# Kernel optimization log

Hardware: AMD Instinct MI355X
Metric: run time of the kernel (lower is better)

The kernel has to match this reference:

```python
import jax, jax.numpy as jnp
import numpy as np

N = 50000      # nodes
E = 800000     # edges (before self-loops)
H = 4          # attention heads
C = 64         # hidden_dim per head
F_IN = 8       # node_features
NEG_SLOPE = 0.2  # PyG GATConv default


def setup_inputs() -> dict:
    key = jax.random.key(0)
    ks = jax.random.split(key, 16)
    def g(k, shape, fan_in):
        return (jax.random.normal(k, shape, jnp.float32) / np.sqrt(fan_in)).astype(jnp.float32)
    x = jax.random.normal(ks[0], (N, F_IN), jnp.float32)
    edge_index = jax.random.randint(ks[1], (2, E), 0, N, dtype=jnp.int32)
    # GATConv params: layer 0 maps F_IN->H*C, layers 1,2 map H*C->H*C
    W0 = g(ks[2], (F_IN, H * C), F_IN)
    Ws = g(ks[3], (2, H * C, H * C), H * C)
    att_src = g(ks[4], (3, H, C), C)
    att_dst = g(ks[5], (3, H, C), C)
    bconv = jnp.zeros((3, H * C), jnp.float32)
    # order / time predictor MLPs: Linear(256,64) -> ReLU -> Linear(64,1)
    ow1 = g(ks[6], (H * C, C), H * C); ob1 = jnp.zeros((C,), jnp.float32)
    ow2 = g(ks[7], (C, 1), C);         ob2 = jnp.zeros((1,), jnp.float32)
    tw1 = g(ks[8], (H * C, C), H * C); tb1 = jnp.zeros((C,), jnp.float32)
    tw2 = g(ks[9], (C, 1), C);         tb2 = jnp.zeros((1,), jnp.float32)
    return {"x": x, "edge_index": edge_index, "W0": W0, "Ws": Ws,
            "att_src": att_src, "att_dst": att_dst, "bconv": bconv,
            "ow1": ow1, "ob1": ob1, "ow2": ow2, "ob2": ob2,
            "tw1": tw1, "tb1": tb1, "tw2": tw2, "tb2": tb2}


def _gat_layer(h_in, src, dst, W, a_src, a_dst, b):
    """PyG-style GATConv (concat heads, eval mode, self-loops already in src/dst)."""
    h = (h_in @ W).reshape(N, H, C)                       # [N,H,C]
    al_s = jnp.einsum('nhc,hc->nh', h, a_src)             # [N,H]
    al_d = jnp.einsum('nhc,hc->nh', h, a_dst)             # [N,H]
    e = jax.nn.leaky_relu(al_s[src] + al_d[dst], NEG_SLOPE)  # [Etot,H]
    m = jax.ops.segment_max(e, dst, num_segments=N)       # segment-softmax over in-edges
    ee = jnp.exp(e - m[dst])
    den = jax.ops.segment_sum(ee, dst, num_segments=N)
    alpha = ee / den[dst]                                 # [Etot,H]
    out = jax.ops.segment_sum(h[src] * alpha[:, :, None], dst, num_segments=N)
    return out.reshape(N, H * C) + b


def reference(x, edge_index, W0, Ws, att_src, att_dst, bconv,
              ow1, ob1, ow2, ob2, tw1, tb1, tw2, tb2):
    loops = jnp.arange(N, dtype=edge_index.dtype)
    src = jnp.concatenate([edge_index[0], loops])
    dst = jnp.concatenate([edge_index[1], loops])
    h = _gat_layer(x, src, dst, W0, att_src[0], att_dst[0], bconv[0])
    h = jax.nn.relu(h)   # dropout is identity in eval
    h = _gat_layer(h, src, dst, Ws[0], att_src[1], att_dst[1], bconv[1])
    h = jax.nn.relu(h)
    h = _gat_layer(h, src, dst, Ws[1], att_src[2], att_dst[2], bconv[2])
    order_scores = jax.nn.relu(h @ ow1 + ob1) @ ow2 + ob2  # [N,1]
    time_scores = jax.nn.relu(h @ tw1 + tb1) @ tw2 + tb2   # [N,1]
    return (order_scores, time_scores)
```

## Files before the change

### kernel.cpp

```cpp
#include <hip/hip_runtime.h>
#include <hip/hip_bf16.h>
#include <hip/hip_fp16.h>

#define NN 50000
#define EE 800000
#define ET 850000
#define HH 4
#define CC 64
#define HC 256

using f16v8 = __attribute__((ext_vector_type(8))) _Float16;
using f32v4 = __attribute__((ext_vector_type(4))) float;

__device__ __forceinline__ float4 cvt_h4(uint2 raw) {
    __half2 a = *reinterpret_cast<__half2*>(&raw.x);
    __half2 b = *reinterpret_cast<__half2*>(&raw.y);
    float2 fa = __half22float2(a), fb = __half22float2(b);
    return make_float4(fa.x, fa.y, fb.x, fb.y);
}

#define HISTB 3321
__global__ void k_hist_prep(const int* __restrict__ ei, int* __restrict__ cnt,
                            const float* __restrict__ Ws,
                            const float* __restrict__ ow1, const float* __restrict__ tw1,
                            __half* __restrict__ Wt, __half* __restrict__ Wh) {
    if (blockIdx.x < HISTB) {
        int e = blockIdx.x * 256 + threadIdx.x;
        if (e < ET) {
            int d = (e < EE) ? ei[EE + e] : (e - EE);
            atomicAdd(&cnt[d], 1);
        }
        return;
    }
    int i = (blockIdx.x - HISTB) * 256 + threadIdx.x;
    if (i < 2 * HC * HC) {
        int m = i >> 16;
        int n = (i >> 8) & 255;
        int k = i & 255;
        Wt[i] = __float2half(Ws[m * HC * HC + k * HC + n]);
    }
    int j = i - 2 * HC * HC;
    if (j >= 0 && j < 128 * HC) {
        int c = j >> 8;
        int k = j & 255;
        float v = (c < 64) ? ow1[k * CC + c] : tw1[k * CC + (c - 64)];
        Wh[j] = __float2half(v);
    }
}

#define ASSIGNB 196
#define G0_NODES 16
__global__ __launch_bounds__(256) void k_assign_gemm0(
        const int* __restrict__ cnt, int* __restrict__ row_ptr,
        int* __restrict__ cur, int* __restrict__ cursor,
        const float* __restrict__ x, const float* __restrict__ W0,
        const float* __restrict__ asrc, const float* __restrict__ adst,
        __half* __restrict__ hg, float* __restrict__ al_s,
        float* __restrict__ al_d) {
    if (blockIdx.x < ASSIGNB) {
        int d = blockIdx.x * 256 + threadIdx.x;
        if (d < NN) {
            int off = atomicAdd(cursor, cnt[d]);
            row_ptr[d] = off;
            cur[d] = off;
        }
        return;
    }
    __shared__ float sx[G0_NODES * 8];
    int t = threadIdx.x;
    int n0 = (blockIdx.x - ASSIGNB) * G0_NODES;
    float w[8];
#pragma unroll
    for (int k = 0; k < 8; k++) w[k] = W0[k * HC + t];
    float as = asrc[t], ad = adst[t];
    int lane = t & 63, wv = t >> 6;
    if (t < G0_NODES * 8) sx[t] = x[(size_t)n0 * 8 + t];
    __syncthreads();
    for (int ni = 0; ni < G0_NODES; ni++) {
        int n = n0 + ni;
        float acc = 0.f;
#pragma unroll
        for (int k = 0; k < 8; k++) acc += sx[ni * 8 + k] * w[k];
        hg[(size_t)n * HC + t] = __float2half(acc);
        float s = acc * as, d = acc * ad;
        for (int off = 32; off > 0; off >>= 1) {
            s += __shfl_down(s, off, 64);
            d += __shfl_down(d, off, 64);
        }
        if (lane == 0) { al_s[n * HH + wv] = s; al_d[n * HH + wv] = d; }
    }
}

__global__ void k_scatter(const int* __restrict__ ei, int* __restrict__ cur,
                          unsigned short* __restrict__ esrc) {
    int e = blockIdx.x * blockDim.x + threadIdx.x;
    if (e < ET) {
        int d, s;
        if (e < EE) { d = ei[EE + e]; s = ei[e]; }
        else        { d = e - EE;     s = d; }
        int pos = atomicAdd(&cur[d], 1);
        esrc[pos] = (unsigned short)s;
    }
}

#define GM 128
#define GN 128
#define GK 64
__global__ __launch_bounds__(256) void k_gemmh(const __half* __restrict__ A,
                                               const __half* __restrict__ Bt,
                                               const float* __restrict__ asrc,
                                               const float* __restrict__ adst,
                                               __half* __restrict__ hg,
                                               float* __restrict__ al_s,
                                               float* __restrict__ al_d) {
    __shared__ __half As[GM][GK + 8];
    __shared__ __half Bs[GN][GK + 8];
    int t = threadIdx.x;
    int l = t & 63, wv = t >> 6;
    int wm = wv >> 1, wn = wv & 1;
    int row0 = blockIdx.x * GM;
    int col0 = blockIdx.y * GN;
    f32v4 acc[4][4] = {};
    const __half* Ab = A + (size_t)row0 * HC;
    const __half* Bb = Bt + (size_t)col0 * HC;
    int sr = t >> 3, sc = (t & 7) * 8;
    for (int k0 = 0; k0 < HC; k0 += GK) {
#pragma unroll
        for (int i = 0; i < 4; i++) {
            int rr = sr + i * 32;
            uint4 v = {0u, 0u, 0u, 0u};
            if (row0 + rr < NN) v = *(const uint4*)(Ab + (size_t)rr * HC + k0 + sc);
            *(uint4*)&As[rr][sc] = v;
            *(uint4*)&Bs[rr][sc] = *(const uint4*)(Bb + (size_t)rr * HC + k0 + sc);
        }
        __syncthreads();
#pragma unroll
        for (int kk = 0; kk < GK; kk += 32) {
            f16v8 af[4], bf[4];
#pragma unroll
            for (int i = 0; i < 4; i++)
                af[i] = *(const f16v8*)&As[wm * 64 + i * 16 + (l & 15)][kk + (l >> 4) * 8];
#pragma unroll
            for (int j = 0; j < 4; j++)
                bf[j] = *(const f16v8*)&Bs[wn * 64 + j * 16 + (l & 15)][kk + (l >> 4) * 8];
#pragma unroll
            for (int i = 0; i < 4; i++)
#pragma unroll
                for (int j = 0; j < 4; j++)
                    acc[i][j] = __builtin_amdgcn_mfma_f32_16x16x32_f16(af[i], bf[j], acc[i][j], 0, 0, 0);
        }
        __syncthreads();
    }
    int head = (col0 >> 6) + wn;
    float va[4], vd[4];
#pragma unroll
    for (int j = 0; j < 4; j++) {
        int c = j * 16 + (l & 15);
        va[j] = asrc[head * CC + c];
        vd[j] = adst[head * CC + c];
    }
    int cbase = col0 + wn * 64 + (l & 15);
#pragma unroll
    for (int i = 0; i < 4; i++) {
#pragma unroll
        for (int v = 0; v < 4; v++) {
            int r = row0 + wm * 64 + i * 16 + (l >> 4) * 4 + v;
            bool ok = (r < NN);
            float s = 0.f, d = 0.f;
#pragma unroll
            for (int j = 0; j < 4; j++) {
                float xv = acc[i][j][v];
                s += xv * va[j];
                d += xv * vd[j];
                if (ok) hg[(size_t)r * HC + cbase + j * 16] = __float2half(xv);
            }
            s += __shfl_xor(s, 8, 16); d += __shfl_xor(d, 8, 16);
            s += __shfl_xor(s, 4, 16); d += __shfl_xor(d, 4, 16);
            s += __shfl_xor(s, 2, 16); d += __shfl_xor(d, 2, 16);
            s += __shfl_xor(s, 1, 16); d += __shfl_xor(d, 1, 16);
            if (ok && (l & 15) == 0) {
                al_s[r * HH + head] = s;
                al_d[r * HH + head] = d;
            }
        }
    }
}

__global__ __launch_bounds__(256) void k_fagg(const int* __restrict__ cnt,
                                              const int* __restrict__ row_ptr,
                                              const unsigned short* __restrict__ esrc,
                                              const float* __restrict__ al_s,
                                              const float* __restrict__ al_d,
                                              const __half* __restrict__ hg,
                                              const float* __restrict__ bias,
                                              __half* __restrict__ out, int do_relu) {
    __shared__ float s_p[4][HH][72];
    __shared__ int   s_src[4][64];
    int t = threadIdx.x;
    int wv = t >> 6, l = t & 63;
    int n = blockIdx.x * 4 + wv;
    int myh = l >> 4;
    int beg = row_ptr[n];
    int end = beg + cnt[n];
    float4 ad = *(const float4*)&al_d[(size_t)n * HH];
    float den = 0.f;
    float4 acc = {0.f, 0.f, 0.f, 0.f};
    const __half* hgl = hg + l * 4;

    for (int off = beg; off < end; off += 64) {
        int csize = min(64, end - off);
        float4 pp = {0.f, 0.f, 0.f, 0.f};
        int s = 0;
        if (l < csize) {
            s = (int)esrc[(size_t)off + l];
            float4 as = *(const float4*)&al_s[(size_t)s * HH];
            float v;
            v = as.x + ad.x; pp.x = __expf((v > 0.f) ? v : 0.2f * v);
            v = as.y + ad.y; pp.y = __expf((v > 0.f) ? v : 0.2f * v);
            v = as.z + ad.z; pp.z = __expf((v > 0.f) ? v : 0.2f * v);
            v = as.w + ad.w; pp.w = __expf((v > 0.f) ? v : 0.2f * v);
        }
        s_src[wv][l] = s;
        s_p[wv][0][l] = pp.x;
        s_p[wv][1][l] = pp.y;
        s_p[wv][2][l] = pp.z;
        s_p[wv][3][l] = pp.w;
        const float* prow = s_p[wv][myh];
        const int*   srow = s_src[wv];
        int k = 0;
        for (; k + 8 <= csize; k += 8) {
            int si[8];
#pragma unroll
            for (int u = 0; u < 8; u++) si[u] = srow[k + u];
            uint2 rw[8];
#pragma unroll
            for (int u = 0; u < 8; u++) rw[u] = *(const uint2*)&hgl[(size_t)si[u] * HC];
            float p[8];
#pragma unroll
            for (int u = 0; u < 8; u++) p[u] = prow[k + u];
#pragma unroll
            for (int u = 0; u < 8; u++) {
                float4 v = cvt_h4(rw[u]);
                den += p[u];
                acc.x += p[u] * v.x;
                acc.y += p[u] * v.y;
                acc.z += p[u] * v.z;
                acc.w += p[u] * v.w;
            }
        }
        for (; k + 4 <= csize; k += 4) {
            int si[4];
#pragma unroll
            for (int u = 0; u < 4; u++) si[u] = srow[k + u];
            uint2 rw[4];
#pragma unroll
            for (int u = 0; u < 4; u++) rw[u] = *(const uint2*)&hgl[(size_t)si[u] * HC];
            float p[4];
#pragma unroll
            for (int u = 0; u < 4; u++) p[u] = prow[k + u];
#pragma unroll
            for (int u = 0; u < 4; u++) {
                float4 v = cvt_h4(rw[u]);
                den += p[u];
                acc.x += p[u] * v.x;
                acc.y += p[u] * v.y;
                acc.z += p[u] * v.z;
                acc.w += p[u] * v.w;
            }
        }
        for (; k < csize; k++) {
            float p = prow[k];
            float4 v = cvt_h4(*(const uint2*)&hgl[(size_t)srow[k] * HC]);
            den += p;
            acc.x += p * v.x; acc.y += p * v.y; acc.z += p * v.z; acc.w += p * v.w;
        }
    }

    float4 b = *(const float4*)&bias[l * 4];
    float inv = 1.f / den;
    float4 o;
    o.x = acc.x * inv + b.x; o.y = acc.y * inv + b.y;
    o.z = acc.z * inv + b.z; o.w = acc.w * inv + b.w;
    if (do_relu) {
        o.x = fmaxf(o.x, 0.f); o.y = fmaxf(o.y, 0.f);
        o.z = fmaxf(o.z, 0.f); o.w = fmaxf(o.w, 0.f);
    }
    union { __half h[4]; uint2 u; } pk;
    pk.h[0] = __float2half(o.x); pk.h[1] = __float2half(o.y);
    pk.h[2] = __float2half(o.z); pk.h[3] = __float2half(o.w);
    *(uint2*)&out[(size_t)n * HC + l * 4] = pk.u;
}

__global__ __launch_bounds__(256) void k_headh(const __half* __restrict__ A,
                                               const __half* __restrict__ Wh,
                                               const float* __restrict__ ob1,
                                               const float* __restrict__ ow2,
                                               const float* __restrict__ ob2,
                                               const float* __restrict__ tb1,
                                               const float* __restrict__ tw2,
                                               const float* __restrict__ tb2,
                                               float* __restrict__ out) {
    __shared__ __half As[GM][GK + 8];
    __shared__ __half Bs[GN][GK + 8];
    int t = threadIdx.x;
    int l = t & 63, wv = t >> 6;
    int wm = wv >> 1, wn = wv & 1;
    int row0 = blockIdx.x * GM;
    f32v4 acc[4][4] = {};
    const __half* Ab = A + (size_t)row0 * HC;
    int sr = t >> 3, sc = (t & 7) * 8;
    for (int k0 = 0; k0 < HC; k0 += GK) {
#pragma unroll
        for (int i = 0; i < 4; i++) {
            int rr = sr + i * 32;
            uint4 v = {0u, 0u, 0u, 0u};
            if (row0 + rr < NN) v = *(const uint4*)(Ab + (size_t)rr * HC + k0 + sc);
            *(uint4*)&As[rr][sc] = v;
            *(uint4*)&Bs[rr][sc] = *(const uint4*)(Wh + (size_t)rr * HC + k0 + sc);
        }
        __syncthreads();
#pragma unroll
        for (int kk = 0; kk < GK; kk += 32) {
            f16v8 af[4], bf[4];
#pragma unroll
            for (int i = 0; i < 4; i++)
                af[i] = *(const f16v8*)&As[wm * 64 + i * 16 + (l & 15)][kk + (l >> 4) * 8];
#pragma unroll
            for (int j = 0; j < 4; j++)
                bf[j] = *(const f16v8*)&Bs[wn * 64 + j * 16 + (l & 15)][kk + (l >> 4) * 8];
#pragma unroll
            for (int i = 0; i < 4; i++)
#pragma unroll
                for (int j = 0; j < 4; j++)
                    acc[i][j] = __builtin_amdgcn_mfma_f32_16x16x32_f16(af[i], bf[j], acc[i][j], 0, 0, 0);
        }
        __syncthreads();
    }
    float b1[4], w2[4];
#pragma unroll
    for (int j = 0; j < 4; j++) {
        int c = j * 16 + (l & 15);
        b1[j] = wn ? tb1[c] : ob1[c];
        w2[j] = wn ? tw2[c] : ow2[c];
    }
    float b2 = wn ? tb2[0] : ob2[0];
#pragma unroll
    for (int i = 0; i < 4; i++) {
#pragma unroll
        for (int v = 0; v < 4; v++) {
            int r = row0 + wm * 64 + i * 16 + (l >> 4) * 4 + v;
            float s = 0.f;
#pragma unroll
            for (int j = 0; j < 4; j++)
                s += fmaxf(acc[i][j][v] + b1[j], 0.f) * w2[j];
            s += __shfl_xor(s, 8, 16);
            s += __shfl_xor(s, 4, 16);
            s += __shfl_xor(s, 2, 16);
            s += __shfl_xor(s, 1, 16);
            if ((l & 15) == 0 && r < NN)
                out[(size_t)(wn ? NN : 0) + r] = s + b2;
        }
    }
}

extern "C" void kernel_launch(void* const* d_in, const int* in_sizes, int n_in,
                              void* d_out, int out_size, void* d_ws, size_t ws_size,
                              hipStream_t stream) {
    const float* x      = (const float*)d_in[0];
    const int*   ei     = (const int*)d_in[1];
    const float* W0     = (const float*)d_in[2];
    const float* Ws     = (const float*)d_in[3];
    const float* attsrc = (const float*)d_in[4];
    const float* attdst = (const float*)d_in[5];
    const float* bconv  = (const float*)d_in[6];
    const float* ow1 = (const float*)d_in[7];
    const float* ob1 = (const float*)d_in[8];
    const float* ow2 = (const float*)d_in[9];
    const float* ob2 = (const float*)d_in[10];
    const float* tw1 = (const float*)d_in[11];
    const float* tb1 = (const float*)d_in[12];
    const float* tw2 = (const float*)d_in[13];
    const float* tb2 = (const float*)d_in[14];
    float* outp = (float*)d_out;

    char* ws = (char*)d_ws;
    size_t off = 0;
    auto alloc = [&](size_t bytes) -> void* {
        void* p = ws + off;
        off += (bytes + 255) & ~(size_t)255;
        return p;
    };
    __half*         hA      = (__half*)alloc(sizeof(__half) * NN * HC);
    __half*         hB16    = (__half*)alloc(sizeof(__half) * NN * HC);
    float*          al_s    = (float*)alloc(sizeof(float) * NN * HH);
    float*          al_d    = (float*)alloc(sizeof(float) * NN * HH);
    int*            cnt     = (int*)alloc(sizeof(int) * NN);
    int*            row_ptr = (int*)alloc(sizeof(int) * NN);
    int*            cur     = (int*)alloc(sizeof(int) * NN);
    int*            cursor  = (int*)alloc(sizeof(int));
    unsigned short* esrc    = (unsigned short*)alloc(sizeof(unsigned short) * ET);
    __half*         Wt      = (__half*)alloc(sizeof(__half) * 2 * HC * HC);
    __half*         Wh      = (__half*)alloc(sizeof(__half) * 128 * HC);
    (void)ws_size; (void)in_sizes; (void)n_in; (void)out_size;

    hipMemsetAsync(cnt, 0, sizeof(int) * NN, stream);
    hipMemsetAsync(cursor, 0, sizeof(int), stream);
    k_hist_prep<<<HISTB + 640, 256, 0, stream>>>(ei, cnt, Ws, ow1, tw1, Wt, Wh);
    k_assign_gemm0<<<ASSIGNB + NN / G0_NODES, 256, 0, stream>>>(
        cnt, row_ptr, cur, cursor, x, W0, attsrc, attdst, hA, al_s, al_d);
    k_scatter<<<(ET + 255) / 256, 256, 0, stream>>>(ei, cur, esrc);

    for (int l = 0; l < 3; l++) {
        if (l > 0) {
            dim3 grid((NN + GM - 1) / GM, 2);
            k_gemmh<<<grid, 256, 0, stream>>>(hB16, Wt + (size_t)(l - 1) * HC * HC,
                                              attsrc + l * HC, attdst + l * HC,
                                              hA, al_s, al_d);
        }
        k_fagg<<<NN / 4, 256, 0, stream>>>(cnt, row_ptr, esrc, al_s, al_d,
                                           hA, bconv + l * HC, hB16,
                                           (l < 2) ? 1 : 0);
    }

    k_headh<<<(NN + GM - 1) / GM, 256, 0, stream>>>(hB16, Wh, ob1, ow2, ob2,
                                                    tb1, tw2, tb2, outp);
}
```

Before: 386.3 us.

## Use full-width 64x256 GEMM tiles and warp-aggregated CSR offset assignment

The hidden-layer GEMM now gives each block 64 rows across all 256 output columns, replacing 128x128 tiles on a two-column grid. Each A tile is read once instead of twice, and each wave reduces attention logits for two heads. In the offset-assignment phase, each wave prefix-sums its counts and issues one atomic instead of one per node, which cuts contention on the global cursor. The cost is a larger shared B tile (256x72 halves), more accumulator registers per thread and more B traffic per block, which may lower occupancy.

```diff
diff --git a/kernel.cpp b/kernel.cpp
--- a/kernel.cpp
+++ b/kernel.cpp
@@ -59,11 +59,20 @@
         float* __restrict__ al_d) {
     if (blockIdx.x < ASSIGNB) {
         int d = blockIdx.x * 256 + threadIdx.x;
-        if (d < NN) {
-            int off = atomicAdd(cursor, cnt[d]);
-            row_ptr[d] = off;
-            cur[d] = off;
-        }
+        int lane = threadIdx.x & 63;
+        int c = (d < NN) ? cnt[d] : 0;
+        int pref = c;
+#pragma unroll
+        for (int o = 1; o < 64; o <<= 1) {
+            int u = __shfl_up(pref, o, 64);
+            if (lane >= o) pref += u;
+        }
+        int tot = __shfl(pref, 63, 64);
+        int base = 0;
+        if (lane == 63) base = atomicAdd(cursor, tot);
+        base = __shfl(base, 63, 64);
+        int off0 = base + pref - c;
+        if (d < NN) { row_ptr[d] = off0; cur[d] = off0; }
         return;
     }
     __shared__ float sx[G0_NODES * 8];
@@ -103,8 +112,7 @@
     }
 }
 
-#define GM 128
-#define GN 128
+#define GM2 64
 #define GK 64
 __global__ __launch_bounds__(256) void k_gemmh(const __half* __restrict__ A,
                                                const __half* __restrict__ Bt,
@@ -113,74 +121,82 @@
                                                __half* __restrict__ hg,
                                                float* __restrict__ al_s,
                                                float* __restrict__ al_d) {
-    __shared__ __half As[GM][GK + 8];
-    __shared__ __half Bs[GN][GK + 8];
+    __shared__ __half As[GM2][GK + 8];
+    __shared__ __half Bs[256][GK + 8];
     int t = threadIdx.x;
     int l = t & 63, wv = t >> 6;
     int wm = wv >> 1, wn = wv & 1;
-    int row0 = blockIdx.x * GM;
-    int col0 = blockIdx.y * GN;
-    f32v4 acc[4][4] = {};
+    int row0 = blockIdx.x * GM2;
+    f32v4 acc[2][8] = {};
     const __half* Ab = A + (size_t)row0 * HC;
-    const __half* Bb = Bt + (size_t)col0 * HC;
-    int sr = t >> 3, sc = (t & 7) * 8;
     for (int k0 = 0; k0 < HC; k0 += GK) {
 #pragma unroll
-        for (int i = 0; i < 4; i++) {
-            int rr = sr + i * 32;
+        for (int i = 0; i < 2; i++) {
+            int idx = t + i * 256;
+            int rr = idx >> 3, c8 = (idx & 7) * 8;
             uint4 v = {0u, 0u, 0u, 0u};
-            if (row0 + rr < NN) v = *(const uint4*)(Ab + (size_t)rr * HC + k0 + sc);
-            *(uint4*)&As[rr][sc] = v;
-            *(uint4*)&Bs[rr][sc] = *(const uint4*)(Bb + (size_t)rr * HC + k0 + sc);
+            if (row0 + rr < NN) v = *(const uint4*)(Ab + (size_t)rr * HC + k0 + c8);
+            *(uint4*)&As[rr][c8] = v;
+        }
+#pragma unroll
+        for (int i = 0; i < 8; i++) {
+            int idx = t + i * 256;
+            int rr = idx >> 3, c8 = (idx & 7) * 8;
+            *(uint4*)&Bs[rr][c8] = *(const uint4*)(Bt + (size_t)rr * HC + k0 + c8);
         }
         __syncthreads();
 #pragma unroll
         for (int kk = 0; kk < GK; kk += 32) {
-            f16v8 af[4], bf[4];
-#pragma unroll
-            for (int i = 0; i < 4; i++)
-                af[i] = *(const f16v8*)&As[wm * 64 + i * 16 + (l & 15)][kk + (l >> 4) * 8];
-#pragma unroll
-            for (int j = 0; j < 4; j++)
-                bf[j] = *(const f16v8*)&Bs[wn * 64 + j * 16 + (l & 15)][kk + (l >> 4) * 8];
-#pragma unroll
-            for (int i = 0; i < 4; i++)
-#pragma unroll
-                for (int j = 0; j < 4; j++)
+            f16v8 af[2], bf[8];
+#pragma unroll
+            for (int i = 0; i < 2; i++)
+                af[i] = *(const f16v8*)&As[wm * 32 + i * 16 + (l & 15)][kk + (l >> 4) * 8];
+#pragma unroll
+            for (int j = 0; j < 8; j++)
+                bf[j] = *(const f16v8*)&Bs[wn * 128 + j * 16 + (l & 15)][kk + (l >> 4) * 8];
+#pragma unroll
+            for (int i = 0; i < 2; i++)
+#pragma unroll
+                for (int j = 0; j < 8; j++)
                     acc[i][j] = __builtin_amdgcn_mfma_f32_16x16x32_f16(af[i], bf[j], acc[i][j], 0, 0, 0);
         }
         __syncthreads();
     }
-    int head = (col0 >> 6) + wn;
-    float va[4], vd[4];
-#pragma unroll
-    for (int j = 0; j < 4; j++) {
-        int c = j * 16 + (l & 15);
-        va[j] = asrc[head * CC + c];
-        vd[j] = adst[head * CC + c];
-    }
-    int cbase = col0 + wn * 64 + (l & 15);
-#pragma unroll
-    for (int i = 0; i < 4; i++) {
+    int h0 = wn * 2;
+    float va[8], vd[8];
+#pragma unroll
+    for (int j = 0; j < 8; j++) {
+        int c = (j & 3) * 16 + (l & 15);
+        int h = h0 + (j >> 2);
+        va[j] = asrc[h * CC + c];
+        vd[j] = adst[h * CC + c];
+    }
+    int cbase = wn * 128 + (l & 15);
+#pragma unroll
+    for (int i = 0; i < 2; i++) {
 #pragma unroll
         for (int v = 0; v < 4; v++) {
-            int r = row0 + wm * 64 + i * 16 + (l >> 4) * 4 + v;
+            int r = row0 + wm * 32 + i * 16 + (l >> 4) * 4 + v;
             bool ok = (r < NN);
-            float s = 0.f, d = 0.f;
-#pragma unroll
-            for (int j = 0; j < 4; j++) {
+            float s0 = 0.f, d0 = 0.f, s1 = 0.f, d1 = 0.f;
+#pragma unroll
+            for (int j = 0; j < 8; j++) {
                 float xv = acc[i][j][v];
-                s += xv * va[j];
-                d += xv * vd[j];
+                if (j < 4) { s0 += xv * va[j]; d0 += xv * vd[j]; }
+                else       { s1 += xv * va[j]; d1 += xv * vd[j]; }
                 if (ok) hg[(size_t)r * HC + cbase + j * 16] = __float2half(xv);
             }
-            s += __shfl_xor(s, 8, 16); d += __shfl_xor(d, 8, 16);
-            s += __shfl_xor(s, 4, 16); d += __shfl_xor(d, 4, 16);
-            s += __shfl_xor(s, 2, 16); d += __shfl_xor(d, 2, 16);
-            s += __shfl_xor(s, 1, 16); d += __shfl_xor(d, 1, 16);
+            s0 += __shfl_xor(s0, 8, 16); d0 += __shfl_xor(d0, 8, 16);
+            s1 += __shfl_xor(s1, 8, 16); d1 += __shfl_xor(d1, 8, 16);
+            s0 += __shfl_xor(s0, 4, 16); d0 += __shfl_xor(d0, 4, 16);
+            s1 += __shfl_xor(s1, 4, 16); d1 += __shfl_xor(d1, 4, 16);
+            s0 += __shfl_xor(s0, 2, 16); d0 += __shfl_xor(d0, 2, 16);
+            s1 += __shfl_xor(s1, 2, 16); d1 += __shfl_xor(d1, 2, 16);
+            s0 += __shfl_xor(s0, 1, 16); d0 += __shfl_xor(d0, 1, 16);
+            s1 += __shfl_xor(s1, 1, 16); d1 += __shfl_xor(d1, 1, 16);
             if (ok && (l & 15) == 0) {
-                al_s[r * HH + head] = s;
-                al_d[r * HH + head] = d;
+                al_s[r * HH + h0] = s0;     al_d[r * HH + h0] = d0;
+                al_s[r * HH + h0 + 1] = s1; al_d[r * HH + h0 + 1] = d1;
             }
         }
     }
@@ -291,6 +307,8 @@
     *(uint2*)&out[(size_t)n * HC + l * 4] = pk.u;
 }
 
+#define GM 128
+#define GN 128
 __global__ __launch_bounds__(256) void k_headh(const __half* __restrict__ A,
                                                const __half* __restrict__ Wh,
                                                const float* __restrict__ ob1,
@@ -412,10 +430,9 @@
 
     for (int l = 0; l < 3; l++) {
         if (l > 0) {
-            dim3 grid((NN + GM - 1) / GM, 2);
-            k_gemmh<<<grid, 256, 0, stream>>>(hB16, Wt + (size_t)(l - 1) * HC * HC,
-                                              attsrc + l * HC, attdst + l * HC,
-                                              hA, al_s, al_d);
+            k_gemmh<<<(NN + GM2 - 1) / GM2, 256, 0, stream>>>(
+                hB16, Wt + (size_t)(l - 1) * HC * HC,
+                attsrc + l * HC, attdst + l * HC, hA, al_s, al_d);
         }
         k_fagg<<<NN / 4, 256, 0, stream>>>(cnt, row_ptr, esrc, al_s, al_d,
                                            hA, bconv + l * HC, hB16,
```

Result: slower. 395.7 us (+2.4%).
